# Kernel tuning notes

Hardware: AMD Instinct MI355X
Metric: run time of the kernel (lower is better)

## Reference

```python
import jax, jax.numpy as jnp
import numpy as np

NUM_USERS, NUM_ITEMS, NUM_GROUPS = 500000, 100000, 100000
D, B, M, F = 64, 1024, 16, 32


def setup_inputs() -> dict:
    key = jax.random.key(0)
    ks = jax.random.split(key, 16)
    def norm(k, shape, scale=0.05):
        return jax.random.normal(k, shape, dtype=jnp.float32) * scale
    return {
        "group_inputs": jax.random.randint(ks[0], (B,), 0, NUM_GROUPS),
        "item_inputs": jax.random.randint(ks[1], (B,), 0, NUM_ITEMS),
        "member_ids": jax.random.randint(ks[2], (B, M), 0, NUM_USERS),
        "follow_ids": jax.random.randint(ks[3], (B, M, F), 0, NUM_USERS),
        "user_table": norm(ks[4], (NUM_USERS, D)),
        "item_table": norm(ks[5], (NUM_ITEMS, D)),
        "group_table": norm(ks[6], (NUM_GROUPS, D)),
        "follow_table": norm(ks[7], (NUM_USERS, D)),
        "fatt_w1": norm(ks[8], (2 * D, 16)), "fatt_b1": jnp.zeros((16,), jnp.float32),
        "fatt_w2": norm(ks[9], (16, 1)), "fatt_b2": jnp.zeros((1,), jnp.float32),
        "att_w1": norm(ks[10], (2 * D, 16)), "att_b1": jnp.zeros((16,), jnp.float32),
        "att_w2": norm(ks[11], (16, 1)), "att_b2": jnp.zeros((1,), jnp.float32),
        "pred_w1": norm(ks[12], (3 * D, 8)), "pred_b1": jnp.zeros((8,), jnp.float32),
        "pred_w2": norm(ks[13], (8, 1)), "pred_b2": jnp.zeros((1,), jnp.float32),
    }


def _att_scores(x, w1, b1, w2, b2):
    # AttentionLayer: Linear(2D,16) -> ReLU -> Linear(16,1); return [..., last MLP axis squeezed]
    h = jax.nn.relu(x @ w1 + b1)
    return (h @ w2 + b2)[..., 0]


def reference(group_inputs, item_inputs, member_ids, follow_ids,
              user_table, item_table, group_table, follow_table,
              fatt_w1, fatt_b1, fatt_w2, fatt_b2,
              att_w1, att_b1, att_w2, att_b2,
              pred_w1, pred_b1, pred_w2, pred_b2):
    # --- user_aggregate: follow-level attention for every member of every group ---
    f_emb = follow_table[follow_ids]                      # [B,M,F,D]
    u_emb = user_table[member_ids]                        # [B,M,D]
    uf = jnp.concatenate(
        [f_emb, jnp.broadcast_to(u_emb[:, :, None, :], f_emb.shape)], axis=-1)  # [B,M,F,2D]
    fw = jax.nn.softmax(_att_scores(uf, fatt_w1, fatt_b1, fatt_w2, fatt_b2), axis=-1)  # [B,M,F]
    members = jnp.einsum('bmf,bmfd->bmd', fw, f_emb) + u_emb                    # [B,M,D]
    # --- group-level (member) attention conditioned on the item ---
    i_emb = item_table[item_inputs]                       # [B,D]
    mi = jnp.concatenate(
        [members, jnp.broadcast_to(i_emb[:, None, :], members.shape)], axis=-1)  # [B,M,2D]
    mw = jax.nn.softmax(_att_scores(mi, att_w1, att_b1, att_w2, att_b2), axis=-1)  # [B,M]
    g_emb = jnp.einsum('bm,bmd->bd', mw, members) + group_table[group_inputs]   # [B,D]
    # --- NCF-style predict head ---
    new = jnp.concatenate([g_emb * i_emb, g_emb, i_emb], axis=-1)               # [B,3D]
    return jax.nn.sigmoid(jax.nn.relu(new @ pred_w1 + pred_b1) @ pred_w2 + pred_b2)  # [B,1]
```

## Files before the change

### kernel.cpp

```cpp
#include <hip/hip_runtime.h>
#include <math.h>


#define TROW 36
#define TMH  (32 * TROW + 16)

__global__ __launch_bounds__(256, 3) void soagree_kernel(
    const int* __restrict__ group_inputs,
    const int* __restrict__ item_inputs,
    const int* __restrict__ member_ids,
    const int* __restrict__ follow_ids,
    const float* __restrict__ user_table,
    const float* __restrict__ item_table,
    const float* __restrict__ group_table,
    const float* __restrict__ follow_table,
    const float* __restrict__ fatt_w1, const float* __restrict__ fatt_b1,
    const float* __restrict__ fatt_w2, const float* __restrict__ fatt_b2,
    const float* __restrict__ att_w1,  const float* __restrict__ att_b1,
    const float* __restrict__ att_w2,  const float* __restrict__ att_b2,
    const float* __restrict__ pred_w1, const float* __restrict__ pred_b1,
    const float* __restrict__ pred_w2, const float* __restrict__ pred_b2,
    float* __restrict__ out)
{
    const int b    = blockIdx.x;
    const int tid  = threadIdx.x;
    const int w    = tid >> 6;
    const int lane = tid & 63;
    const int f    = lane & 31;
    const int mh   = lane >> 5;

    __shared__ float s_tile[4][2 * TMH];
    __shared__ float s_uemb[16][65];
    __shared__ float s_mem[16][65];
    __shared__ float s_upart[16][16];
    __shared__ float s_ipart[16];
    __shared__ float s_iemb[64];
    __shared__ float s_gemb[64];
    __shared__ float s_gfin[64];
    __shared__ float s_scores[16];
    __shared__ float s_mw[16];

    if (tid < 64) {
        s_iemb[tid] = item_table[(size_t)item_inputs[b] * 64 + tid];
    } else if (tid < 128) {
        s_gemb[tid - 64] = group_table[(size_t)group_inputs[b] * 64 + (tid - 64)];
    }
    for (int m = w; m < 16; m += 4) {
        int uid = member_ids[b * 16 + m];
        s_uemb[m][lane] = user_table[(size_t)uid * 64 + lane];
    }
    __syncthreads();

    {
        int m = tid >> 4, j = tid & 15;
        float acc = fatt_b1[j];
        #pragma unroll
        for (int d = 0; d < 64; ++d)
            acc += s_uemb[m][d] * fatt_w1[(64 + d) * 16 + j];
        s_upart[m][j] = acc;
    }
    if (tid < 16) {
        float a2 = att_b1[tid];
        #pragma unroll
        for (int d = 0; d < 64; ++d)
            a2 += s_iemb[d] * att_w1[(64 + d) * 16 + tid];
        s_ipart[tid] = a2;
    }
    __syncthreads();

    float* const tw_base = &s_tile[w][0];

    #pragma unroll
    for (int pr = 0; pr < 2; ++pr) {
        const int pb = w * 4 + pr * 2;
        const int m  = pb + mh;

        const int fid = follow_ids[b * 512 + pb * 32 + lane];
        const float4* src = (const float4*)(follow_table + (size_t)fid * 64);
        float4 r[16];
        #pragma unroll
        for (int q = 0; q < 16; ++q) r[q] = src[q];

        float hacc[16];
        #pragma unroll
        for (int jj = 0; jj < 4; ++jj) {
            float4 up = *(const float4*)&s_upart[m][jj * 4];
            hacc[jj * 4 + 0] = up.x; hacc[jj * 4 + 1] = up.y;
            hacc[jj * 4 + 2] = up.z; hacc[jj * 4 + 3] = up.w;
        }

        const float* rf = (const float*)r;
        #pragma unroll
        for (int d = 0; d < 64; ++d) {
            const float v = rf[d];
            #pragma unroll
            for (int j = 0; j < 16; ++j)
                hacc[j] += v * fatt_w1[d * 16 + j];
        }
        float sc = fatt_b2[0];
        #pragma unroll
        for (int j = 0; j < 16; ++j)
            sc += fmaxf(hacc[j], 0.f) * fatt_w2[j];

        float mx = sc;
        #pragma unroll
        for (int mk = 16; mk >= 1; mk >>= 1) mx = fmaxf(mx, __shfl_xor(mx, mk));
        const float e = __expf(sc - mx);
        float se = e;
        #pragma unroll
        for (int mk = 16; mk >= 1; mk >>= 1) se += __shfl_xor(se, mk);
        const float fwv = e / se;

        float* const tw = tw_base + mh * TMH + f * TROW;

        #pragma unroll
        for (int q = 0; q < 8; ++q) {
            float4 sr;
            sr.x = r[q].x * fwv; sr.y = r[q].y * fwv;
            sr.z = r[q].z * fwv; sr.w = r[q].w * fwv;
            *(float4*)&tw[q * 4] = sr;
        }
        asm volatile("s_waitcnt lgkmcnt(0)" ::: "memory");
        __builtin_amdgcn_sched_barrier(0);
        {
            float acc = s_uemb[m][f];
            #pragma unroll
            for (int ff = 0; ff < 32; ++ff)
                acc += tw_base[mh * TMH + ff * TROW + f];
            s_mem[m][f] = acc;
        }
        asm volatile("s_waitcnt lgkmcnt(0)" ::: "memory");
        __builtin_amdgcn_sched_barrier(0);

        #pragma unroll
        for (int q = 8; q < 16; ++q) {
            float4 sr;
            sr.x = r[q].x * fwv; sr.y = r[q].y * fwv;
            sr.z = r[q].z * fwv; sr.w = r[q].w * fwv;
            *(float4*)&tw[(q - 8) * 4] = sr;
        }
        asm volatile("s_waitcnt lgkmcnt(0)" ::: "memory");
        __builtin_amdgcn_sched_barrier(0);
        {
            float acc = s_uemb[m][f + 32];
            #pragma unroll
            for (int ff = 0; ff < 32; ++ff)
                acc += tw_base[mh * TMH + ff * TROW + f];
            s_mem[m][f + 32] = acc;
        }
        asm volatile("s_waitcnt lgkmcnt(0)" ::: "memory");
        __builtin_amdgcn_sched_barrier(0);
    }
    __syncthreads();

    {
        int m = tid >> 4, j = tid & 15;
        float acc = s_ipart[j];
        #pragma unroll
        for (int d = 0; d < 64; ++d)
            acc += s_mem[m][d] * att_w1[d * 16 + j];
        float contrib = fmaxf(acc, 0.f) * att_w2[j];
        #pragma unroll
        for (int mk = 8; mk >= 1; mk >>= 1) contrib += __shfl_xor(contrib, mk);
        if (j == 0) s_scores[m] = contrib + att_b2[0];
    }
    __syncthreads();
    if (tid < 16) {
        float s = s_scores[tid];
        float mx2 = s;
        #pragma unroll
        for (int mk = 8; mk >= 1; mk >>= 1) mx2 = fmaxf(mx2, __shfl_xor(mx2, mk));
        float e2 = __expf(s - mx2);
        float sm2 = e2;
        #pragma unroll
        for (int mk = 8; mk >= 1; mk >>= 1) sm2 += __shfl_xor(sm2, mk);
        s_mw[tid] = e2 / sm2;
    }
    __syncthreads();
    if (tid < 64) {
        float g = s_gemb[tid];
        #pragma unroll
        for (int mm = 0; mm < 16; ++mm)
            g += s_mw[mm] * s_mem[mm][tid];
        s_gfin[tid] = g;
    }
    __syncthreads();

    if (tid < 8) {
        const int j = tid;
        float acc = pred_b1[j];
        #pragma unroll 16
        for (int k = 0; k < 64; ++k) {
            float g = s_gfin[k], ie = s_iemb[k];
            acc += (g * ie) * pred_w1[k * 8 + j];
            acc += g  * pred_w1[(64 + k) * 8 + j];
            acc += ie * pred_w1[(128 + k) * 8 + j];
        }
        float contrib = fmaxf(acc, 0.f) * pred_w2[j];
        #pragma unroll
        for (int mk = 4; mk >= 1; mk >>= 1) contrib += __shfl_xor(contrib, mk);
        if (j == 0) {
            float z = contrib + pred_b2[0];
            out[b] = 1.f / (1.f + __expf(-z));
        }
    }
}

extern "C" void kernel_launch(void* const* d_in, const int* in_sizes, int n_in,
                              void* d_out, int out_size, void* d_ws, size_t ws_size,
                              hipStream_t stream) {
    const int*   group_inputs = (const int*)d_in[0];
    const int*   item_inputs  = (const int*)d_in[1];
    const int*   member_ids   = (const int*)d_in[2];
    const int*   follow_ids   = (const int*)d_in[3];
    const float* user_table   = (const float*)d_in[4];
    const float* item_table   = (const float*)d_in[5];
    const float* group_table  = (const float*)d_in[6];
    const float* follow_table = (const float*)d_in[7];
    const float* fatt_w1 = (const float*)d_in[8];
    const float* fatt_b1 = (const float*)d_in[9];
    const float* fatt_w2 = (const float*)d_in[10];
    const float* fatt_b2 = (const float*)d_in[11];
    const float* att_w1  = (const float*)d_in[12];
    const float* att_b1  = (const float*)d_in[13];
    const float* att_w2  = (const float*)d_in[14];
    const float* att_b2  = (const float*)d_in[15];
    const float* pred_w1 = (const float*)d_in[16];
    const float* pred_b1 = (const float*)d_in[17];
    const float* pred_w2 = (const float*)d_in[18];
    const float* pred_b2 = (const float*)d_in[19];
    float* outp = (float*)d_out;

    const int B = in_sizes[0];

    soagree_kernel<<<B, 256, 0, stream>>>(
        group_inputs, item_inputs, member_ids, follow_ids,
        user_table, item_table, group_table, follow_table,
        fatt_w1, fatt_b1, fatt_w2, fatt_b2,
        att_w1, att_b1, att_w2, att_b2,
        pred_w1, pred_b1, pred_w2, pred_b2,
        outp);
}
```

Baseline: 53.86 us.

## Replace LDS transpose reduction with shuffle butterfly reduce-scatter, raise occupancy

The follow-weighted sum over the 32 follows was done by writing scaled rows to a padded shared-memory tile and having each lane sum a column. It is now done in registers with a five-step butterfly of cross-lane xor shuffles, after which each lane holds two output dimensions. Dropping the roughly 37 KB shared tile frees LDS, so launch bounds are raised to 4 blocks per CU. This targets more in-flight gathers and hides latency better, at the cost of about 62 cross-lane shuffle ops per pass and possible register pressure at the higher occupancy target.

```diff
diff --git a/kernel.cpp b/kernel.cpp
--- a/kernel.cpp
+++ b/kernel.cpp
@@ -2,10 +2,7 @@
 #include <math.h>
 
 
-#define TROW 36
-#define TMH  (32 * TROW + 16)
-
-__global__ __launch_bounds__(256, 3) void soagree_kernel(
+__global__ __launch_bounds__(256, 4) void soagree_kernel(
     const int* __restrict__ group_inputs,
     const int* __restrict__ item_inputs,
     const int* __restrict__ member_ids,
@@ -29,9 +26,8 @@
     const int f    = lane & 31;
     const int mh   = lane >> 5;
 
-    __shared__ float s_tile[4][2 * TMH];
-    __shared__ float s_uemb[16][65];
-    __shared__ float s_mem[16][65];
+    __shared__ float s_uemb[16][66];
+    __shared__ float s_mem[16][66];
     __shared__ float s_upart[16][16];
     __shared__ float s_ipart[16];
     __shared__ float s_iemb[64];
@@ -68,8 +64,6 @@
     }
     __syncthreads();
 
-    float* const tw_base = &s_tile[w][0];
-
     #pragma unroll
     for (int pr = 0; pr < 2; ++pr) {
         const int pb = w * 4 + pr * 2;
@@ -77,9 +71,10 @@
 
         const int fid = follow_ids[b * 512 + pb * 32 + lane];
         const float4* src = (const float4*)(follow_table + (size_t)fid * 64);
-        float4 r[16];
-        #pragma unroll
-        for (int q = 0; q < 16; ++q) r[q] = src[q];
+        float4 r4[16];
+        #pragma unroll
+        for (int q = 0; q < 16; ++q) r4[q] = src[q];
+        float* rf = (float*)r4;
 
         float hacc[16];
         #pragma unroll
@@ -89,7 +84,6 @@
             hacc[jj * 4 + 2] = up.z; hacc[jj * 4 + 3] = up.w;
         }
 
-        const float* rf = (const float*)r;
         #pragma unroll
         for (int d = 0; d < 64; ++d) {
             const float v = rf[d];
@@ -111,45 +105,30 @@
         for (int mk = 16; mk >= 1; mk >>= 1) se += __shfl_xor(se, mk);
         const float fwv = e / se;
 
-        float* const tw = tw_base + mh * TMH + f * TROW;
-
-        #pragma unroll
-        for (int q = 0; q < 8; ++q) {
-            float4 sr;
-            sr.x = r[q].x * fwv; sr.y = r[q].y * fwv;
-            sr.z = r[q].z * fwv; sr.w = r[q].w * fwv;
-            *(float4*)&tw[q * 4] = sr;
-        }
-        asm volatile("s_waitcnt lgkmcnt(0)" ::: "memory");
-        __builtin_amdgcn_sched_barrier(0);
-        {
-            float acc = s_uemb[m][f];
-            #pragma unroll
-            for (int ff = 0; ff < 32; ++ff)
-                acc += tw_base[mh * TMH + ff * TROW + f];
-            s_mem[m][f] = acc;
-        }
-        asm volatile("s_waitcnt lgkmcnt(0)" ::: "memory");
-        __builtin_amdgcn_sched_barrier(0);
-
-        #pragma unroll
-        for (int q = 8; q < 16; ++q) {
-            float4 sr;
-            sr.x = r[q].x * fwv; sr.y = r[q].y * fwv;
-            sr.z = r[q].z * fwv; sr.w = r[q].w * fwv;
-            *(float4*)&tw[(q - 8) * 4] = sr;
-        }
-        asm volatile("s_waitcnt lgkmcnt(0)" ::: "memory");
-        __builtin_amdgcn_sched_barrier(0);
-        {
-            float acc = s_uemb[m][f + 32];
-            #pragma unroll
-            for (int ff = 0; ff < 32; ++ff)
-                acc += tw_base[mh * TMH + ff * TROW + f];
-            s_mem[m][f + 32] = acc;
-        }
-        asm volatile("s_waitcnt lgkmcnt(0)" ::: "memory");
-        __builtin_amdgcn_sched_barrier(0);
+        #pragma unroll
+        for (int d = 0; d < 64; ++d) rf[d] *= fwv;
+
+        #define BSTEP(M, S)                                                  \
+        {                                                                    \
+            const bool hi = (lane & (M)) != 0;                               \
+            _Pragma("unroll")                                                \
+            for (int k = 0; k < (S) / 2; ++k) {                              \
+                float send = hi ? rf[k] : rf[k + (S) / 2];                   \
+                float recv = __shfl_xor(send, (M));                          \
+                float keep = hi ? rf[k + (S) / 2] : rf[k];                   \
+                rf[k] = keep + recv;                                         \
+            }                                                                \
+        }
+        BSTEP(16, 64)
+        BSTEP(8, 32)
+        BSTEP(4, 16)
+        BSTEP(2, 8)
+        BSTEP(1, 4)
+        #undef BSTEP
+
+        float2 ue = *(const float2*)&s_uemb[m][2 * f];
+        float2 res; res.x = rf[0] + ue.x; res.y = rf[1] + ue.y;
+        *(float2*)&s_mem[m][2 * f] = res;
     }
     __syncthreads();
 
```

Result: slower. 108.4 us (+101.3%).
